# Kernel optimization log

Measured on AMD Instinct MI355X. Metric: run time of the kernel, lower is better.

## Reference

```python
import math
import jax, jax.numpy as jnp
import numpy as np

FEATURE_DIM = 16
HEADS = 8
DIM = 512
HEAD_DIM = DIM // HEADS
EPS = 1e-12
_RD = math.sqrt(FEATURE_DIM)        # sqrt(d)
_RRD = math.sqrt(_RD)               # d^{1/4}
_R2 = math.sqrt(2.0)
_IU, _JU = np.triu_indices(FEATURE_DIM, k=1)  # row-major upper-tri (excl diag), matches torch.triu_indices


def taylor_feature_map(x):
    # x: (..., F) -> (..., 1 + F + F + F*(F-1)/2) = (..., 153) for F=16
    off = x[..., _IU] * x[..., _JU]          # upper triangle of outer product, no full FxF materialization
    diag = x * x
    return jnp.concatenate([
        jnp.ones_like(x[..., :1]),
        x / _RRD,
        diag / (_RD * _R2),
        off / _RD,
    ], axis=-1)


def setup_inputs() -> dict:
    key = jax.random.key(0)
    k0, k1, k2, k3, k4 = jax.random.split(key, 5)
    b, t, d = 2, 1024, DIM
    hidden_states = jax.random.normal(k0, (b, t, d), dtype=jnp.float32)
    s = 0.02
    Wq = jax.random.normal(k1, (HEADS * FEATURE_DIM, d), dtype=jnp.float32) * s
    Wk = jax.random.normal(k2, (HEADS * FEATURE_DIM, d), dtype=jnp.float32) * s
    Wv = jax.random.normal(k3, (HEADS * HEAD_DIM, d), dtype=jnp.float32) * s
    Wo = jax.random.normal(k4, (d, HEADS * HEAD_DIM), dtype=jnp.float32) * s
    return {"hidden_states": hidden_states, "Wq": Wq, "Wk": Wk, "Wv": Wv, "Wo": Wo}


def reference(hidden_states, Wq, Wk, Wv, Wo):
    b, t, d = hidden_states.shape
    h, f, hd = HEADS, FEATURE_DIM, HEAD_DIM
    q = (hidden_states @ Wq.T).reshape(b, t, h, f).transpose(0, 2, 1, 3)    # (b,h,t,f)
    k = (hidden_states @ Wk.T).reshape(b, t, h, f).transpose(0, 2, 1, 3)
    v = (hidden_states @ Wv.T).reshape(b, t, h, hd).transpose(0, 2, 1, 3)   # (b,h,t,hd)
    q = taylor_feature_map(q)   # (b,h,t,F) with F=153
    k = taylor_feature_map(k)
    # causal linear attention via cumulative state
    kv = k[..., None, :] * v[..., :, None]          # (b,h,t,hd,F)
    kv_cum = jnp.cumsum(kv, axis=2)                 # (b,h,t,hd,F)
    num = jnp.einsum('bhtf,bhtdf->bhtd', q, kv_cum) # (b,h,t,hd)
    k_cum = jnp.cumsum(k, axis=2)                   # (b,h,t,F)
    den = jnp.einsum('bhtf,bhtf->bht', q, k_cum)[..., None] + EPS
    y = num / den                                   # (b,h,t,hd)
    y = y.transpose(0, 2, 1, 3).reshape(b, t, h * hd)
    return y @ Wo.T
```

## Files before the change

kernel.cpp:

```cpp
#include <hip/hip_runtime.h>
#include <hip/hip_bf16.h>

#define BB 2
#define TT 1024
#define DD 512
#define HH 8
#define FF 16
#define HDIM 64
#define BT (BB*TT)

typedef short bf16x8 __attribute__((ext_vector_type(8)));
typedef float f32x4  __attribute__((ext_vector_type(4)));
#define MFMA_BF16 __builtin_amdgcn_mfma_f32_16x16x32_bf16

__device__ __forceinline__ ushort f2b(float f) {
    uint u = __float_as_uint(f);
    uint r = (u + 0x7fffu + ((u >> 16) & 1u)) >> 16;
    return (ushort)r;
}

__device__ __forceinline__ uint pkbf2(float a, float b) {
    __hip_bfloat162 h = __float22bfloat162_rn(make_float2(a, b));
    union { __hip_bfloat162 h2; uint u; } c; c.h2 = h;
    return c.u;
}

__global__ __launch_bounds__(256) void cast_all(
    const float* __restrict__ X,  const float* __restrict__ Wq,
    const float* __restrict__ Wk, const float* __restrict__ Wv,
    const float* __restrict__ Wo,
    ushort* __restrict__ Xb, ushort* __restrict__ Wb, ushort* __restrict__ Wob)
{
    const int i4 = (blockIdx.x * 256 + threadIdx.x) * 4;
    const float* src; ushort* dst;
    if (i4 < 1048576)      { src = X  + i4;             dst = Xb + i4; }
    else if (i4 < 1114112) { src = Wq + (i4 - 1048576); dst = Wb + (i4 - 1048576); }
    else if (i4 < 1179648) { src = Wk + (i4 - 1114112); dst = Wb + 65536 + (i4 - 1114112); }
    else if (i4 < 1441792) { src = Wv + (i4 - 1179648); dst = Wb + 131072 + (i4 - 1179648); }
    else                   { src = Wo + (i4 - 1441792); dst = Wob + (i4 - 1441792); }
    float4 v = *(const float4*)src;
    ushort4 o = { f2b(v.x), f2b(v.y), f2b(v.z), f2b(v.w) };
    *(ushort4*)dst = o;
}

__global__ __launch_bounds__(512) void qkv_mfma(
    const ushort* __restrict__ Xb, const ushort* __restrict__ Wb,
    ushort* __restrict__ Qb, ushort* __restrict__ Kb, ushort* __restrict__ Vtg)
{
    __shared__ float sc[2][64][66];
    const int m0 = blockIdx.x * 64, n0 = blockIdx.y * 64;
    const int tid = threadIdx.x, w = tid >> 6, l = tid & 63;
    const int kw = w >> 2, mw = w & 1, nw = (w >> 1) & 1;
    const int lr = l & 15, g = l >> 4;

    f32x4 acc[2][2] = {};
    const ushort* Ar = Xb + (size_t)(m0 + mw*32 + lr) * 512 + kw*256 + g*8;
    const ushort* Br = Wb + (size_t)(n0 + nw*32 + lr) * 512 + kw*256 + g*8;

    bf16x8 a0c = *(const bf16x8*)(Ar);
    bf16x8 a1c = *(const bf16x8*)(Ar + (size_t)16*512);
    bf16x8 b0c = *(const bf16x8*)(Br);
    bf16x8 b1c = *(const bf16x8*)(Br + (size_t)16*512);
    #pragma unroll
    for (int ks = 0; ks < 8; ++ks) {
        bf16x8 a0n = a0c, a1n = a1c, b0n = b0c, b1n = b1c;
        if (ks < 7) {
            a0n = *(const bf16x8*)(Ar + (ks+1)*32);
            a1n = *(const bf16x8*)(Ar + (size_t)16*512 + (ks+1)*32);
            b0n = *(const bf16x8*)(Br + (ks+1)*32);
            b1n = *(const bf16x8*)(Br + (size_t)16*512 + (ks+1)*32);
        }
        acc[0][0] = MFMA_BF16(a0c, b0c, acc[0][0], 0, 0, 0);
        acc[0][1] = MFMA_BF16(a0c, b1c, acc[0][1], 0, 0, 0);
        acc[1][0] = MFMA_BF16(a1c, b0c, acc[1][0], 0, 0, 0);
        acc[1][1] = MFMA_BF16(a1c, b1c, acc[1][1], 0, 0, 0);
        a0c = a0n; a1c = a1n; b0c = b0n; b1c = b1n;
    }

    #pragma unroll
    for (int mb = 0; mb < 2; ++mb)
        #pragma unroll
        for (int nb = 0; nb < 2; ++nb)
            #pragma unroll
            for (int r = 0; r < 4; ++r)
                sc[kw][mw*32 + mb*16 + g*4 + r][nw*32 + nb*16 + lr] = acc[mb][nb][r];
    __syncthreads();

    const int vl = tid & 63, rg = tid >> 6;
    const int cg = n0 + vl;
    float v8[8];
    #pragma unroll
    for (int j = 0; j < 8; ++j) v8[j] = sc[0][rg*8 + j][vl] + sc[1][rg*8 + j][vl];
    const int tok0 = m0 + rg*8;
    const int b = tok0 >> 10, tt0 = tok0 & 1023;
    if (cg < 256) {
        const bool isQ = cg < 128;
        const int c = isQ ? cg : cg - 128;
        const int h = c >> 4, f = c & 15;
        ushort* Dst = isQ ? Qb : Kb;
        const float scale = isQ ? 1.0f : 0.25f;
        #pragma unroll
        for (int j = 0; j < 8; ++j)
            Dst[((size_t)(b*HH + h)*TT + tt0 + j)*FF + f] = f2b(v8[j] * scale);
    } else {
        const int c = cg - 256;
        const int h = c >> 6, v = c & 63;
        uint2 p0 = { pkbf2(v8[0], v8[1]), pkbf2(v8[2], v8[3]) };
        uint2 p1 = { pkbf2(v8[4], v8[5]), pkbf2(v8[6], v8[7]) };
        ushort* base = Vtg + ((size_t)(b*HH + h)*64 + v)*TT + tt0;
        *(uint2*)base       = p0;
        *(uint2*)(base + 4) = p1;
    }
}

__global__ __launch_bounds__(512) void attn_mfma(
    const ushort* __restrict__ Qb, const ushort* __restrict__ Kb,
    const ushort* __restrict__ Vtg, ushort* __restrict__ Yb)
{
    __shared__ float smem[8*32*68 + 8*32];
    short (*Pl)[32][72] = (short(*)[32][72])smem;
    float* scf = smem;
    float* scd = smem + 8*32*68;

    const int bid = blockIdx.x;
    const int qt = 31 - (bid >> 4);
    const int bh = bid & 15;
    const int b = bh >> 3, h = bh & 7;
    const int tid = threadIdx.x, w = tid >> 6, l = tid & 63;
    const int lr = l & 15, g = l >> 4;
    const int qend = qt*32 + 32;
    const int nkc = (qt + 2) >> 1;
    const bf16x8 zf = {0,0,0,0,0,0,0,0};
    const bf16x8 ones = {16256,16256,16256,16256,16256,16256,16256,16256};

    bf16x8 qf[2];
    #pragma unroll
    for (int nb = 0; nb < 2; ++nb)
        qf[nb] = (l < 32)
            ? *(const bf16x8*)(Qb + ((size_t)bh*TT + qt*32 + nb*16 + lr)*FF + g*8)
            : zf;

    f32x4 o[4][2] = {};
    f32x4 dacc[2] = {};

    for (int kc = w; kc < nkc; kc += 8) {
        const bool diagc = (kc == nkc - 1);
        const int act = qend - kc*64;
        const int nmb = diagc ? (act >> 4) : 4;
        const int kb_max = nmb >> 1;

        for (int mb = 0; mb < nmb; ++mb) {
            bf16x8 kf = (l < 32)
                ? *(const bf16x8*)(Kb + ((size_t)bh*TT + kc*64 + mb*16 + lr)*FF + g*8)
                : zf;
            #pragma unroll
            for (int nb = 0; nb < 2; ++nb) {
                f32x4 z4 = {};
                f32x4 s = MFMA_BF16(kf, qf[nb], z4, 0, 0, 0);
                float pv[4];
                if (diagc) {
                    const int qg = qt*32 + nb*16 + lr;
                    const int kg0 = kc*64 + mb*16 + g*4;
                    #pragma unroll
                    for (int r = 0; r < 4; ++r) {
                        float pp = fmaf(s[r], fmaf(s[r], 0.5f, 1.0f), 1.0f);
                        pv[r] = (kg0 + r > qg) ? 0.f : pp;
                    }
                } else {
                    #pragma unroll
                    for (int r = 0; r < 4; ++r)
                        pv[r] = fmaf(s[r], fmaf(s[r], 0.5f, 1.0f), 1.0f);
                }
                uint2 pk = { pkbf2(pv[0], pv[1]), pkbf2(pv[2], pv[3]) };
                *(uint2*)&Pl[w][nb*16 + lr][mb*16 + g*4] = pk;
            }
        }

        for (int kb = 0; kb < kb_max; ++kb) {
            #pragma unroll
            for (int mv = 0; mv < 4; ++mv) {
                bf16x8 vf = *(const bf16x8*)(Vtg +
                    ((size_t)bh*64 + mv*16 + lr)*TT + kc*64 + kb*32 + g*8);
                #pragma unroll
                for (int nb = 0; nb < 2; ++nb) {
                    bf16x8 pf = *(const bf16x8*)&Pl[w][nb*16 + lr][kb*32 + g*8];
                    o[mv][nb] = MFMA_BF16(vf, pf, o[mv][nb], 0, 0, 0);
                }
            }
            #pragma unroll
            for (int nb = 0; nb < 2; ++nb) {
                bf16x8 pf = *(const bf16x8*)&Pl[w][nb*16 + lr][kb*32 + g*8];
                dacc[nb] = MFMA_BF16(ones, pf, dacc[nb], 0, 0, 0);
            }
        }
    }

    __syncthreads();

    #pragma unroll
    for (int mv = 0; mv < 4; ++mv)
        #pragma unroll
        for (int nb = 0; nb < 2; ++nb)
            *(f32x4*)&scf[(size_t)(w*32 + nb*16 + lr)*68 + mv*16 + g*4] = o[mv][nb];
    if (g == 0) {
        scd[w*32 + lr]      = dacc[0][0];
        scd[w*32 + 16 + lr] = dacc[1][0];
    }

    __syncthreads();

    {
        const int q  = tid >> 4;
        const int v0 = (tid & 15) * 4;
        float dtot = 0.f;
        #pragma unroll
        for (int ww = 0; ww < 8; ++ww) dtot += scd[ww*32 + q];
        const float inv = 1.0f / (dtot + 1e-12f);
        float o0 = 0.f, o1 = 0.f, o2 = 0.f, o3 = 0.f;
        #pragma unroll
        for (int ww = 0; ww < 8; ++ww) {
            const float* p = &scf[(size_t)(ww*32 + q)*68 + v0];
            o0 += p[0]; o1 += p[1]; o2 += p[2]; o3 += p[3];
        }
        uint2 pk = { pkbf2(o0*inv, o1*inv), pkbf2(o2*inv, o3*inv) };
        *(uint2*)(Yb + ((size_t)(b*TT + qt*32 + q))*DD + h*HDIM + v0) = pk;
    }
}

__global__ __launch_bounds__(512) void out_mfma(
    const ushort* __restrict__ Yb, const ushort* __restrict__ Wob,
    float* __restrict__ Out)
{
    __shared__ float sc[2][64][66];
    const int m0 = blockIdx.x * 64, n0 = blockIdx.y * 64;
    const int tid = threadIdx.x, w = tid >> 6, l = tid & 63;
    const int kw = w >> 2, mw = w & 1, nw = (w >> 1) & 1;
    const int lr = l & 15, g = l >> 4;

    f32x4 acc[2][2] = {};
    const ushort* Ar = Yb  + (size_t)(m0 + mw*32 + lr) * 512 + kw*256 + g*8;
    const ushort* Br = Wob + (size_t)(n0 + nw*32 + lr) * 512 + kw*256 + g*8;

    bf16x8 a0c = *(const bf16x8*)(Ar);
    bf16x8 a1c = *(const bf16x8*)(Ar + (size_t)16*512);
    bf16x8 b0c = *(const bf16x8*)(Br);
    bf16x8 b1c = *(const bf16x8*)(Br + (size_t)16*512);
    #pragma unroll
    for (int ks = 0; ks < 8; ++ks) {
        bf16x8 a0n = a0c, a1n = a1c, b0n = b0c, b1n = b1c;
        if (ks < 7) {
            a0n = *(const bf16x8*)(Ar + (ks+1)*32);
            a1n = *(const bf16x8*)(Ar + (size_t)16*512 + (ks+1)*32);
            b0n = *(const bf16x8*)(Br + (ks+1)*32);
            b1n = *(const bf16x8*)(Br + (size_t)16*512 + (ks+1)*32);
        }
        acc[0][0] = MFMA_BF16(a0c, b0c, acc[0][0], 0, 0, 0);
        acc[0][1] = MFMA_BF16(a0c, b1c, acc[0][1], 0, 0, 0);
        acc[1][0] = MFMA_BF16(a1c, b0c, acc[1][0], 0, 0, 0);
        acc[1][1] = MFMA_BF16(a1c, b1c, acc[1][1], 0, 0, 0);
        a0c = a0n; a1c = a1n; b0c = b0n; b1c = b1n;
    }

    #pragma unroll
    for (int mb = 0; mb < 2; ++mb)
        #pragma unroll
        for (int nb = 0; nb < 2; ++nb)
            #pragma unroll
            for (int r = 0; r < 4; ++r)
                sc[kw][mw*32 + mb*16 + g*4 + r][nw*32 + nb*16 + lr] = acc[mb][nb][r];
    __syncthreads();

    const int vl = tid & 63, rg = tid >> 6;
    #pragma unroll
    for (int j = 0; j < 8; ++j) {
        const float v = sc[0][rg*8 + j][vl] + sc[1][rg*8 + j][vl];
        Out[(size_t)(m0 + rg*8 + j)*512 + n0 + vl] = v;
    }
}

extern "C" void kernel_launch(void* const* d_in, const int* in_sizes, int n_in,
                              void* d_out, int out_size, void* d_ws, size_t ws_size,
                              hipStream_t stream) {
    const float* X  = (const float*)d_in[0];
    const float* Wq = (const float*)d_in[1];
    const float* Wk = (const float*)d_in[2];
    const float* Wv = (const float*)d_in[3];
    const float* Wo = (const float*)d_in[4];
    float* out = (float*)d_out;

    ushort* ws = (ushort*)d_ws;
    ushort* Xb  = ws;
    ushort* Wb  = Xb  + 1048576;
    ushort* Wob = Wb  + 393216;
    ushort* Qb  = Wob + 262144;
    ushort* Kb  = Qb  + 262144;
    ushort* Vtg = Kb  + 262144;
    ushort* Yb  = Vtg + 1048576;

    cast_all<<<1664, 256, 0, stream>>>(X, Wq, Wk, Wv, Wo, Xb, Wb, Wob);

    dim3 g1(BT/64, 768/64);
    qkv_mfma<<<g1, 512, 0, stream>>>(Xb, Wb, Qb, Kb, Vtg);

    attn_mfma<<<512, 512, 0, stream>>>(Qb, Kb, Vtg, Yb);

    dim3 g3(BT/64, DD/64);
    out_mfma<<<g3, 512, 0, stream>>>(Yb, Wob, out);
}
```

Baseline: 47.75 us.

## Fuse fp32-to-bf16 cast into QKV GEMM with LDS-tiled 128x128 blocks

Removes the separate cast kernel. The QKV projection now reads fp32 X and weights directly, converts them to bf16 while staging into LDS, and computes 128x128 output tiles per block. An extra grid row converts Wo to bf16 alongside the GEMM. This saves one kernel launch and the round trip of writing and re-reading the bf16 copy of X. The cost is a grid of only 112 blocks, each running a synchronous load-then-compute loop with no prefetch, so latency hiding may suffer.

```diff
diff --git a/kernel.cpp b/kernel.cpp
--- a/kernel.cpp
+++ b/kernel.cpp
@@ -25,91 +25,104 @@
     return c.u;
 }
 
-__global__ __launch_bounds__(256) void cast_all(
+__global__ __launch_bounds__(512) void qkv_f32(
     const float* __restrict__ X,  const float* __restrict__ Wq,
     const float* __restrict__ Wk, const float* __restrict__ Wv,
     const float* __restrict__ Wo,
-    ushort* __restrict__ Xb, ushort* __restrict__ Wb, ushort* __restrict__ Wob)
+    ushort* __restrict__ Qb, ushort* __restrict__ Kb,
+    ushort* __restrict__ Vtg, ushort* __restrict__ Wob)
 {
-    const int i4 = (blockIdx.x * 256 + threadIdx.x) * 4;
-    const float* src; ushort* dst;
-    if (i4 < 1048576)      { src = X  + i4;             dst = Xb + i4; }
-    else if (i4 < 1114112) { src = Wq + (i4 - 1048576); dst = Wb + (i4 - 1048576); }
-    else if (i4 < 1179648) { src = Wk + (i4 - 1114112); dst = Wb + 65536 + (i4 - 1114112); }
-    else if (i4 < 1441792) { src = Wv + (i4 - 1179648); dst = Wb + 131072 + (i4 - 1179648); }
-    else                   { src = Wo + (i4 - 1441792); dst = Wob + (i4 - 1441792); }
-    float4 v = *(const float4*)src;
-    ushort4 o = { f2b(v.x), f2b(v.y), f2b(v.z), f2b(v.w) };
-    *(ushort4*)dst = o;
-}
-
-__global__ __launch_bounds__(512) void qkv_mfma(
-    const ushort* __restrict__ Xb, const ushort* __restrict__ Wb,
-    ushort* __restrict__ Qb, ushort* __restrict__ Kb, ushort* __restrict__ Vtg)
-{
-    __shared__ float sc[2][64][66];
-    const int m0 = blockIdx.x * 64, n0 = blockIdx.y * 64;
+    if (blockIdx.y == 6) {
+        const int idx = blockIdx.x * 512 + threadIdx.x;
+        #pragma unroll
+        for (int j = 0; j < 8; ++j) {
+            const int u = j * 8192 + idx;
+            float4 v = *(const float4*)(Wo + (size_t)u * 4);
+            ushort4 o = { f2b(v.x), f2b(v.y), f2b(v.z), f2b(v.w) };
+            *(ushort4*)(Wob + (size_t)u * 4) = o;
+        }
+        return;
+    }
+
+    __shared__ short LA[128][136];
+    __shared__ short LB[128][136];
+
+    const int m0 = blockIdx.x * 128;
+    const int by = blockIdx.y;
     const int tid = threadIdx.x, w = tid >> 6, l = tid & 63;
-    const int kw = w >> 2, mw = w & 1, nw = (w >> 1) & 1;
+    const int mw = w & 3, nw = w >> 2;
     const int lr = l & 15, g = l >> 4;
 
-    f32x4 acc[2][2] = {};
-    const ushort* Ar = Xb + (size_t)(m0 + mw*32 + lr) * 512 + kw*256 + g*8;
-    const ushort* Br = Wb + (size_t)(n0 + nw*32 + lr) * 512 + kw*256 + g*8;
-
-    bf16x8 a0c = *(const bf16x8*)(Ar);
-    bf16x8 a1c = *(const bf16x8*)(Ar + (size_t)16*512);
-    bf16x8 b0c = *(const bf16x8*)(Br);
-    bf16x8 b1c = *(const bf16x8*)(Br + (size_t)16*512);
-    #pragma unroll
-    for (int ks = 0; ks < 8; ++ks) {
-        bf16x8 a0n = a0c, a1n = a1c, b0n = b0c, b1n = b1c;
-        if (ks < 7) {
-            a0n = *(const bf16x8*)(Ar + (ks+1)*32);
-            a1n = *(const bf16x8*)(Ar + (size_t)16*512 + (ks+1)*32);
-            b0n = *(const bf16x8*)(Br + (ks+1)*32);
-            b1n = *(const bf16x8*)(Br + (size_t)16*512 + (ks+1)*32);
-        }
-        acc[0][0] = MFMA_BF16(a0c, b0c, acc[0][0], 0, 0, 0);
-        acc[0][1] = MFMA_BF16(a0c, b1c, acc[0][1], 0, 0, 0);
-        acc[1][0] = MFMA_BF16(a1c, b0c, acc[1][0], 0, 0, 0);
-        acc[1][1] = MFMA_BF16(a1c, b1c, acc[1][1], 0, 0, 0);
-        a0c = a0n; a1c = a1n; b0c = b0n; b1c = b1n;
-    }
-
-    #pragma unroll
-    for (int mb = 0; mb < 2; ++mb)
-        #pragma unroll
-        for (int nb = 0; nb < 2; ++nb)
-            #pragma unroll
-            for (int r = 0; r < 4; ++r)
-                sc[kw][mw*32 + mb*16 + g*4 + r][nw*32 + nb*16 + lr] = acc[mb][nb][r];
-    __syncthreads();
-
-    const int vl = tid & 63, rg = tid >> 6;
-    const int cg = n0 + vl;
-    float v8[8];
-    #pragma unroll
-    for (int j = 0; j < 8; ++j) v8[j] = sc[0][rg*8 + j][vl] + sc[1][rg*8 + j][vl];
-    const int tok0 = m0 + rg*8;
-    const int b = tok0 >> 10, tt0 = tok0 & 1023;
-    if (cg < 256) {
-        const bool isQ = cg < 128;
-        const int c = isQ ? cg : cg - 128;
-        const int h = c >> 4, f = c & 15;
-        ushort* Dst = isQ ? Qb : Kb;
-        const float scale = isQ ? 1.0f : 0.25f;
-        #pragma unroll
-        for (int j = 0; j < 8; ++j)
-            Dst[((size_t)(b*HH + h)*TT + tt0 + j)*FF + f] = f2b(v8[j] * scale);
+    const float* Wsrc = (by == 0) ? Wq
+                      : (by == 1) ? Wk
+                      : (Wv + (size_t)(by - 2) * 128 * 512);
+
+    f32x4 acc[2][4] = {};
+
+    for (int kc = 0; kc < 4; ++kc) {
+        __syncthreads();
+        #pragma unroll
+        for (int i = 0; i < 8; ++i) {
+            const int f = i * 512 + tid;
+            const int row = f >> 5, c4 = f & 31;
+            float4 va = *(const float4*)(X + (size_t)(m0 + row) * 512 + kc*128 + c4*4);
+            uint2 pa = { pkbf2(va.x, va.y), pkbf2(va.z, va.w) };
+            *(uint2*)&LA[row][c4*4] = pa;
+            float4 vb = *(const float4*)(Wsrc + (size_t)row * 512 + kc*128 + c4*4);
+            uint2 pb = { pkbf2(vb.x, vb.y), pkbf2(vb.z, vb.w) };
+            *(uint2*)&LB[row][c4*4] = pb;
+        }
+        __syncthreads();
+
+        #pragma unroll
+        for (int ks = 0; ks < 4; ++ks) {
+            bf16x8 a0 = *(const bf16x8*)&LA[mw*32      + lr][ks*32 + g*8];
+            bf16x8 a1 = *(const bf16x8*)&LA[mw*32 + 16 + lr][ks*32 + g*8];
+            bf16x8 b0 = *(const bf16x8*)&LB[nw*64      + lr][ks*32 + g*8];
+            bf16x8 b1 = *(const bf16x8*)&LB[nw*64 + 16 + lr][ks*32 + g*8];
+            bf16x8 b2 = *(const bf16x8*)&LB[nw*64 + 32 + lr][ks*32 + g*8];
+            bf16x8 b3 = *(const bf16x8*)&LB[nw*64 + 48 + lr][ks*32 + g*8];
+            acc[0][0] = MFMA_BF16(a0, b0, acc[0][0], 0, 0, 0);
+            acc[0][1] = MFMA_BF16(a0, b1, acc[0][1], 0, 0, 0);
+            acc[0][2] = MFMA_BF16(a0, b2, acc[0][2], 0, 0, 0);
+            acc[0][3] = MFMA_BF16(a0, b3, acc[0][3], 0, 0, 0);
+            acc[1][0] = MFMA_BF16(a1, b0, acc[1][0], 0, 0, 0);
+            acc[1][1] = MFMA_BF16(a1, b1, acc[1][1], 0, 0, 0);
+            acc[1][2] = MFMA_BF16(a1, b2, acc[1][2], 0, 0, 0);
+            acc[1][3] = MFMA_BF16(a1, b3, acc[1][3], 0, 0, 0);
+        }
+    }
+
+    if (by < 2) {
+        ushort* Dst = (by == 0) ? Qb : Kb;
+        const float scale = (by == 0) ? 1.0f : 0.25f;
+        #pragma unroll
+        for (int mb = 0; mb < 2; ++mb)
+            #pragma unroll
+            for (int nb = 0; nb < 4; ++nb) {
+                const int n = nw*64 + nb*16 + lr;
+                const int h = n >> 4, fc = n & 15;
+                #pragma unroll
+                for (int r = 0; r < 4; ++r) {
+                    const int tok = m0 + mw*32 + mb*16 + g*4 + r;
+                    const int b = tok >> 10, tt = tok & 1023;
+                    Dst[((size_t)(b*HH + h)*TT + tt)*FF + fc] =
+                        f2b(acc[mb][nb][r] * scale);
+                }
+            }
     } else {
-        const int c = cg - 256;
-        const int h = c >> 6, v = c & 63;
-        uint2 p0 = { pkbf2(v8[0], v8[1]), pkbf2(v8[2], v8[3]) };
-        uint2 p1 = { pkbf2(v8[4], v8[5]), pkbf2(v8[6], v8[7]) };
-        ushort* base = Vtg + ((size_t)(b*HH + h)*64 + v)*TT + tt0;
-        *(uint2*)base       = p0;
-        *(uint2*)(base + 4) = p1;
+        #pragma unroll
+        for (int mb = 0; mb < 2; ++mb)
+            #pragma unroll
+            for (int nb = 0; nb < 4; ++nb) {
+                const int n = (by - 2)*128 + nw*64 + nb*16 + lr;
+                const int h = n >> 6, v = n & 63;
+                const int tok0 = m0 + mw*32 + mb*16 + g*4;
+                const int b = tok0 >> 10, tt0 = tok0 & 1023;
+                uint2 pk = { pkbf2(acc[mb][nb][0], acc[mb][nb][1]),
+                             pkbf2(acc[mb][nb][2], acc[mb][nb][3]) };
+                *(uint2*)&Vtg[((size_t)(b*HH + h)*64 + v)*TT + tt0] = pk;
+            }
     }
 }
 
@@ -289,18 +302,14 @@
     float* out = (float*)d_out;
 
     ushort* ws = (ushort*)d_ws;
-    ushort* Xb  = ws;
-    ushort* Wb  = Xb  + 1048576;
-    ushort* Wob = Wb  + 393216;
+    ushort* Wob = ws;
     ushort* Qb  = Wob + 262144;
     ushort* Kb  = Qb  + 262144;
     ushort* Vtg = Kb  + 262144;
     ushort* Yb  = Vtg + 1048576;
 
-    cast_all<<<1664, 256, 0, stream>>>(X, Wq, Wk, Wv, Wo, Xb, Wb, Wob);
-
-    dim3 g1(BT/64, 768/64);
-    qkv_mfma<<<g1, 512, 0, stream>>>(Xb, Wb, Qb, Kb, Vtg);
+    dim3 g1(16, 7);
+    qkv_f32<<<g1, 512, 0, stream>>>(X, Wq, Wk, Wv, Wo, Qb, Kb, Vtg, Wob);
 
     attn_mfma<<<512, 512, 0, stream>>>(Qb, Kb, Vtg, Yb);
 
```

Result: faster. 43.07 us (median of 2 runs) (-9.8%).
